# Optimization experiments

Measured on AMD Instinct MI355X. Metric: run time of the kernel, lower is better.

## Reference

```python
import jax, jax.numpy as jnp
import numpy as np

B, T, C, H = 8, 1024, 1024, 16  # batch, seq, n_embd, n_head


def setup_inputs() -> dict:
    key = jax.random.key(0)
    ks = jax.random.split(key, 5)
    scale = 1.0 / np.sqrt(C)
    return {
        "x": jax.random.normal(ks[0], (B, T, C), dtype=jnp.float32),
        "Wqkv": jax.random.normal(ks[1], (C, 3 * C), dtype=jnp.float32) * scale,
        "bqkv": jax.random.normal(ks[2], (3 * C,), dtype=jnp.float32) * 0.02,
        "Wproj": jax.random.normal(ks[3], (C, C), dtype=jnp.float32) * scale,
        "bproj": jax.random.normal(ks[4], (C,), dtype=jnp.float32) * 0.02,
        "n_head": H,
    }


def reference(x, Wqkv, bqkv, Wproj, bproj, n_head):
    Bb, Tt, Cc = x.shape
    hd = Cc // n_head  # head dim
    qkv = x @ Wqkv + bqkv                      # [B,T,3C]
    q, k, v = jnp.split(qkv, 3, axis=-1)       # each [B,T,C]
    # [B,T,C] -> [B,H,T,hd]
    def to_heads(t):
        return t.reshape(Bb, Tt, n_head, hd).transpose(0, 2, 1, 3)
    q, k, v = to_heads(q), to_heads(k), to_heads(v)
    scores = jnp.einsum("bhqd,bhkd->bhqk", q, k) / jnp.sqrt(jnp.asarray(hd, q.dtype))
    causal = jnp.tril(jnp.ones((Tt, Tt), dtype=bool))
    scores = jnp.where(causal, scores, jnp.asarray(-jnp.inf, scores.dtype))
    attn = jax.nn.softmax(scores, axis=-1)
    y = jnp.einsum("bhqk,bhkd->bhqd", attn, v)  # [B,H,T,hd]
    y = y.transpose(0, 2, 1, 3).reshape(Bb, Tt, Cc)
    return y @ Wproj + bproj
```

## Files before the change

kernel.cpp:

```cpp
#include <hip/hip_runtime.h>
#include <math.h>

#define Bz 8
#define Tz 1024
#define Cz 1024
#define Hz 16
#define HDz 64
#define Mz (Bz*Tz)
#define N1 (3*Cz)

typedef __attribute__((ext_vector_type(8))) short short8;
typedef __attribute__((ext_vector_type(4))) short short4v;
typedef __attribute__((ext_vector_type(4))) float floatx4;

__device__ __forceinline__ unsigned short f2bf(float f) {
    unsigned u = __float_as_uint(f);
    return (unsigned short)((u + 0x7FFFu + ((u >> 16) & 1u)) >> 16);
}

__device__ __forceinline__ void gload16(const void* g, void* l) {
    __builtin_amdgcn_global_load_lds(
        (const __attribute__((address_space(1))) unsigned int*)g,
        (__attribute__((address_space(3))) unsigned int*)l, 16, 0, 0);
}

__global__ __launch_bounds__(256) void cvt_kernel(const float* __restrict__ src,
    unsigned short* __restrict__ dst, int n4)
{
    int i = blockIdx.x * blockDim.x + threadIdx.x;
    if (i >= n4) return;
    float4 v = *(const float4*)&src[(size_t)i * 4];
    ushort4 o;
    o.x = f2bf(v.x); o.y = f2bf(v.y); o.z = f2bf(v.z); o.w = f2bf(v.w);
    *(ushort4*)&dst[(size_t)i * 4] = o;
}

__global__ __launch_bounds__(256) void wtrans_kernel(const float* __restrict__ W,
    unsigned short* __restrict__ Wt, int K, int N)
{
    __shared__ float tile[32][33];
    const int n0 = blockIdx.x * 32, k0 = blockIdx.y * 32;
    const int tx = threadIdx.x, ty = threadIdx.y;
#pragma unroll
    for (int i = 0; i < 4; ++i)
        tile[ty + i * 8][tx] = W[(size_t)(k0 + ty + i * 8) * N + n0 + tx];
    __syncthreads();
#pragma unroll
    for (int i = 0; i < 4; ++i)
        Wt[(size_t)(n0 + ty + i * 8) * K + k0 + tx] = f2bf(tile[tx][ty + i * 8]);
}

__global__ __launch_bounds__(256) void vtrans_kernel(const unsigned short* __restrict__ qkvb,
    unsigned short* __restrict__ Vt)
{
    __shared__ unsigned short tile[64][72];
    const int t0 = blockIdx.x * 64;
    const int bh = blockIdx.y;
    const int b = bh >> 4, h = bh & 15;
    const int tid = threadIdx.x;
#pragma unroll
    for (int it = 0; it < 2; ++it) {
        int idx = tid + it * 256;
        int tl = idx >> 3, d8 = idx & 7;
        *(short8*)&tile[tl][d8 * 8] =
            *(const short8*)&qkvb[(size_t)(b * Tz + t0 + tl) * N1 + 2 * Cz + h * HDz + d8 * 8];
    }
    __syncthreads();
#pragma unroll
    for (int it = 0; it < 2; ++it) {
        int idx = tid + it * 256;
        int d = idx >> 3, t8 = idx & 7;
        unsigned short o[8];
#pragma unroll
        for (int j = 0; j < 8; ++j) o[j] = tile[t8 * 8 + j][d];
        *(short8*)&Vt[(size_t)bh * (HDz * Tz) + (size_t)d * Tz + t0 + t8 * 8] = *(short8*)o;
    }
}

__global__ __launch_bounds__(256) void gemm_kernel(const unsigned short* __restrict__ A,
    const unsigned short* __restrict__ Bt, const float* __restrict__ bias,
    void* __restrict__ Cout, int M, int N, int K, int outBf16)
{
    __shared__ unsigned short As[128 * 64];
    __shared__ unsigned short Bs[128 * 64];
    const int tid = threadIdx.x;
    const int lane = tid & 63;
    const int w = tid >> 6, wr = w >> 1, wc = w & 1;
    const int quad = lane >> 4, m16 = lane & 15;
    const int row0 = blockIdx.y * 128, col0 = blockIdx.x * 128;

    float bv[4];
#pragma unroll
    for (int ni = 0; ni < 4; ++ni)
        bv[ni] = bias[col0 + wc * 64 + ni * 16 + m16];

    floatx4 acc[4][4];
#pragma unroll
    for (int mi = 0; mi < 4; ++mi)
#pragma unroll
        for (int ni = 0; ni < 4; ++ni)
            acc[mi][ni] = (floatx4){0.f, 0.f, 0.f, 0.f};

    const int l3 = lane >> 3;
    const int swz = ((lane & 7) ^ l3) * 8;
    const unsigned short* gA[4];
    const unsigned short* gB[4];
    unsigned short* lA[4];
    unsigned short* lB[4];
#pragma unroll
    for (int i = 0; i < 4; ++i) {
        int c = w * 4 + i;
        gA[i] = A  + (size_t)(row0 + c * 8 + l3) * K + swz;
        gB[i] = Bt + (size_t)(col0 + c * 8 + l3) * K + swz;
        lA[i] = &As[c * 512];
        lB[i] = &Bs[c * 512];
    }
    const int sw7 = m16 & 7;

    for (int k0 = 0; k0 < K; k0 += 64) {
#pragma unroll
        for (int i = 0; i < 4; ++i) {
            gload16(gA[i] + k0, lA[i]);
            gload16(gB[i] + k0, lB[i]);
        }
        __syncthreads();
#pragma unroll
        for (int s = 0; s < 2; ++s) {
            short8 af[4], bfr[4];
            const int ch = ((s * 4 + quad) ^ sw7) * 8;
#pragma unroll
            for (int mi = 0; mi < 4; ++mi)
                af[mi] = *(short8*)&As[(wr * 64 + mi * 16 + m16) * 64 + ch];
#pragma unroll
            for (int ni = 0; ni < 4; ++ni)
                bfr[ni] = *(short8*)&Bs[(wc * 64 + ni * 16 + m16) * 64 + ch];
#pragma unroll
            for (int mi = 0; mi < 4; ++mi)
#pragma unroll
                for (int ni = 0; ni < 4; ++ni)
                    acc[mi][ni] = __builtin_amdgcn_mfma_f32_16x16x32_bf16(af[mi], bfr[ni], acc[mi][ni], 0, 0, 0);
        }
        __syncthreads();
    }

#pragma unroll
    for (int mi = 0; mi < 4; ++mi)
#pragma unroll
        for (int ni = 0; ni < 4; ++ni)
#pragma unroll
            for (int reg = 0; reg < 4; ++reg) {
                int r = row0 + wr * 64 + mi * 16 + quad * 4 + reg;
                int c = col0 + wc * 64 + ni * 16 + m16;
                float v = acc[mi][ni][reg] + bv[ni];
                if (outBf16) ((unsigned short*)Cout)[(size_t)r * N + c] = f2bf(v);
                else         ((float*)Cout)[(size_t)r * N + c] = v;
            }
}

__global__ __launch_bounds__(256, 3) void attn_kernel(const unsigned short* __restrict__ qkvb,
    const unsigned short* __restrict__ VtG, unsigned short* __restrict__ attb)
{
    __shared__ unsigned short Ks[2][64 * 64];
    __shared__ unsigned short Vs[2][64 * 64];

    const int qi = (int)gridDim.x - 1 - (int)blockIdx.x;
    const int bh = blockIdx.y;
    const int b = bh >> 4, h = bh & 15;
    const int tid = threadIdx.x, lane = tid & 63, w = tid >> 6;
    const int quad = lane >> 4, m16 = lane & 15;
    const int kimax   = 2 * qi + 1;
    const int kimax_w = 2 * qi + (w >> 1);

    const unsigned short* Kb = qkvb + (size_t)(b * Tz) * N1 + Cz + h * HDz;
    const unsigned short* Vb = VtG + (size_t)bh * (HDz * Tz);

    short8 qf[2][2];
    int qrow[2];
#pragma unroll
    for (int mi = 0; mi < 2; ++mi) {
        qrow[mi] = qi * 128 + w * 32 + mi * 16 + m16;
        const size_t rq = (size_t)(b * Tz + qrow[mi]) * N1 + h * HDz;
        qf[mi][0] = *(const short8*)&qkvb[rq + quad * 8];
        qf[mi][1] = *(const short8*)&qkvb[rq + 32 + quad * 8];
    }

    floatx4 of[2][4];
#pragma unroll
    for (int mi = 0; mi < 2; ++mi)
#pragma unroll
        for (int dc = 0; dc < 4; ++dc) of[mi][dc] = (floatx4){0.f, 0.f, 0.f, 0.f};
    float psum[2] = {0.f, 0.f};

    const int l3 = lane >> 3, l7 = lane & 7;
    const int gsw = ((l7 ^ l3) << 3);
    const int r0 = w * 16 + l3, r1 = w * 16 + 8 + l3;
    const int sw = m16 & 7;
    const int p0 = (quad ^ sw) << 3;

    gload16(Kb + (size_t)r0 * N1 + gsw, &Ks[0][(2 * w) * 512]);
    gload16(Kb + (size_t)r1 * N1 + gsw, &Ks[0][(2 * w + 1) * 512]);
    gload16(Vb + (size_t)r0 * Tz + gsw, &Vs[0][(2 * w) * 512]);
    gload16(Vb + (size_t)r1 * Tz + gsw, &Vs[0][(2 * w + 1) * 512]);

    int buf = 0;
    for (int ki = 0; ki <= kimax; ++ki) {
        __syncthreads();
        if (ki < kimax) {
            int kn = (ki + 1) * 64;
            gload16(Kb + (size_t)(kn + r0) * N1 + gsw, &Ks[buf ^ 1][(2 * w) * 512]);
            gload16(Kb + (size_t)(kn + r1) * N1 + gsw, &Ks[buf ^ 1][(2 * w + 1) * 512]);
            gload16(Vb + (size_t)r0 * Tz + kn + gsw, &Vs[buf ^ 1][(2 * w) * 512]);
            gload16(Vb + (size_t)r1 * Tz + kn + gsw, &Vs[buf ^ 1][(2 * w + 1) * 512]);
        }
        if (ki <= kimax_w) {
            short8 pf[2][2];
#pragma unroll
            for (int m0 = 0; m0 < 4; ++m0) {
                const unsigned short* kr = &Ks[buf][(m0 * 16 + m16) * 64];
                short8 kf0 = *(const short8*)&kr[p0];
                short8 kf1 = *(const short8*)&kr[p0 ^ 32];
#pragma unroll
                for (int mi = 0; mi < 2; ++mi) {
                    floatx4 st = (floatx4){0.f, 0.f, 0.f, 0.f};
                    st = __builtin_amdgcn_mfma_f32_16x16x32_bf16(kf0, qf[mi][0], st, 0, 0, 0);
                    st = __builtin_amdgcn_mfma_f32_16x16x32_bf16(kf1, qf[mi][1], st, 0, 0, 0);
                    const bool needm = (ki * 64 + 63) > (qi * 128 + w * 32 + mi * 16);
#pragma unroll
                    for (int reg = 0; reg < 4; ++reg) {
                        float p = exp2f(st[reg] * 0.18033688f);
                        if (needm) {
                            int key = ki * 64 + m0 * 16 + quad * 4 + reg;
                            p = (key <= qrow[mi]) ? p : 0.f;
                        }
                        psum[mi] += p;
                        pf[mi][m0 >> 1][(m0 & 1) * 4 + reg] = (short)f2bf(p);
                    }
                }
            }
#pragma unroll
            for (int dc = 0; dc < 4; ++dc) {
                const unsigned short* vrow = &Vs[buf][(dc * 16 + m16) * 64];
#pragma unroll
                for (int kg = 0; kg < 2; ++kg) {
                    const int g0 = kg * 4 + (quad >> 1);
                    const int off = (quad & 1) * 4;
                    short4v v0 = *(const short4v*)&vrow[((g0 ^ sw) << 3) + off];
                    short4v v1 = *(const short4v*)&vrow[(((g0 + 2) ^ sw) << 3) + off];
                    short8 vf;
                    vf[0] = v0[0]; vf[1] = v0[1]; vf[2] = v0[2]; vf[3] = v0[3];
                    vf[4] = v1[0]; vf[5] = v1[1]; vf[6] = v1[2]; vf[7] = v1[3];
#pragma unroll
                    for (int mi = 0; mi < 2; ++mi)
                        of[mi][dc] = __builtin_amdgcn_mfma_f32_16x16x32_bf16(vf, pf[mi][kg], of[mi][dc], 0, 0, 0);
                }
            }
        }
        buf ^= 1;
    }

#pragma unroll
    for (int mi = 0; mi < 2; ++mi) {
        float l = psum[mi];
        l += __shfl_xor(l, 16);
        l += __shfl_xor(l, 32);
        const float inv = 1.f / l;
        const size_t orow = (size_t)(b * Tz + qrow[mi]) * Cz + h * HDz;
#pragma unroll
        for (int dc = 0; dc < 4; ++dc) {
            ushort4 o;
            o.x = f2bf(of[mi][dc][0] * inv);
            o.y = f2bf(of[mi][dc][1] * inv);
            o.z = f2bf(of[mi][dc][2] * inv);
            o.w = f2bf(of[mi][dc][3] * inv);
            *(ushort4*)&attb[orow + dc * 16 + quad * 4] = o;
        }
    }
}

extern "C" void kernel_launch(void* const* d_in, const int* in_sizes, int n_in,
                              void* d_out, int out_size, void* d_ws, size_t ws_size,
                              hipStream_t stream)
{
    const float* x     = (const float*)d_in[0];
    const float* Wqkv  = (const float*)d_in[1];
    const float* bqkv  = (const float*)d_in[2];
    const float* Wproj = (const float*)d_in[3];
    const float* bproj = (const float*)d_in[4];
    float* out = (float*)d_out;

    unsigned short* xb     = (unsigned short*)d_ws;
    unsigned short* Wqkvt  = xb + (size_t)Mz * Cz;
    unsigned short* Wprojt = Wqkvt + (size_t)N1 * Cz;
    unsigned short* qkvb   = Wprojt + (size_t)Cz * Cz;
    unsigned short* VtG    = qkvb + (size_t)Mz * N1;
    unsigned short* attb   = VtG + (size_t)(Bz * Hz) * HDz * Tz;

    cvt_kernel<<<(Mz * Cz / 4) / 256, 256, 0, stream>>>(x, xb, Mz * Cz / 4);
    wtrans_kernel<<<dim3(N1 / 32, Cz / 32), dim3(32, 8), 0, stream>>>(Wqkv, Wqkvt, Cz, N1);
    wtrans_kernel<<<dim3(Cz / 32, Cz / 32), dim3(32, 8), 0, stream>>>(Wproj, Wprojt, Cz, Cz);

    gemm_kernel<<<dim3(N1 / 128, Mz / 128), 256, 0, stream>>>(
        xb, Wqkvt, bqkv, qkvb, Mz, N1, Cz, 1);

    vtrans_kernel<<<dim3(Tz / 64, Bz * Hz), 256, 0, stream>>>(qkvb, VtG);

    attn_kernel<<<dim3(Tz / 128, Bz * Hz), 256, 0, stream>>>(qkvb, VtG, attb);

    gemm_kernel<<<dim3(Cz / 128, Mz / 128), 256, 0, stream>>>(
        attb, Wprojt, bproj, out, Mz, Cz, Cz, 0);
}
```

Baseline: 281.3 us.

## Pair complementary causal query tiles per block for balanced attention work

```diff
diff --git a/kernel.cpp b/kernel.cpp
--- a/kernel.cpp
+++ b/kernel.cpp
@@ -157,39 +157,21 @@
             }
 }
 
-__global__ __launch_bounds__(256, 3) void attn_kernel(const unsigned short* __restrict__ qkvb,
+__global__ __launch_bounds__(256) void attn_kernel(const unsigned short* __restrict__ qkvb,
     const unsigned short* __restrict__ VtG, unsigned short* __restrict__ attb)
 {
     __shared__ unsigned short Ks[2][64 * 64];
     __shared__ unsigned short Vs[2][64 * 64];
 
-    const int qi = (int)gridDim.x - 1 - (int)blockIdx.x;
+    const int bx = blockIdx.x;
     const int bh = blockIdx.y;
     const int b = bh >> 4, h = bh & 15;
     const int tid = threadIdx.x, lane = tid & 63, w = tid >> 6;
     const int quad = lane >> 4, m16 = lane & 15;
-    const int kimax   = 2 * qi + 1;
-    const int kimax_w = 2 * qi + (w >> 1);
+    const int qis[2] = {15 - bx, bx};
 
     const unsigned short* Kb = qkvb + (size_t)(b * Tz) * N1 + Cz + h * HDz;
     const unsigned short* Vb = VtG + (size_t)bh * (HDz * Tz);
-
-    short8 qf[2][2];
-    int qrow[2];
-#pragma unroll
-    for (int mi = 0; mi < 2; ++mi) {
-        qrow[mi] = qi * 128 + w * 32 + mi * 16 + m16;
-        const size_t rq = (size_t)(b * Tz + qrow[mi]) * N1 + h * HDz;
-        qf[mi][0] = *(const short8*)&qkvb[rq + quad * 8];
-        qf[mi][1] = *(const short8*)&qkvb[rq + 32 + quad * 8];
-    }
-
-    floatx4 of[2][4];
-#pragma unroll
-    for (int mi = 0; mi < 2; ++mi)
-#pragma unroll
-        for (int dc = 0; dc < 4; ++dc) of[mi][dc] = (floatx4){0.f, 0.f, 0.f, 0.f};
-    float psum[2] = {0.f, 0.f};
 
     const int l3 = lane >> 3, l7 = lane & 7;
     const int gsw = ((l7 ^ l3) << 3);
@@ -203,40 +185,50 @@
     gload16(Vb + (size_t)r1 * Tz + gsw, &Vs[0][(2 * w + 1) * 512]);
 
     int buf = 0;
-    for (int ki = 0; ki <= kimax; ++ki) {
-        __syncthreads();
-        if (ki < kimax) {
-            int kn = (ki + 1) * 64;
-            gload16(Kb + (size_t)(kn + r0) * N1 + gsw, &Ks[buf ^ 1][(2 * w) * 512]);
-            gload16(Kb + (size_t)(kn + r1) * N1 + gsw, &Ks[buf ^ 1][(2 * w + 1) * 512]);
-            gload16(Vb + (size_t)r0 * Tz + kn + gsw, &Vs[buf ^ 1][(2 * w) * 512]);
-            gload16(Vb + (size_t)r1 * Tz + kn + gsw, &Vs[buf ^ 1][(2 * w + 1) * 512]);
-        }
-        if (ki <= kimax_w) {
-            short8 pf[2][2];
+    for (int t = 0; t < 2; ++t) {
+        const int qi = qis[t];
+        const int qrow = qi * 64 + w * 16 + m16;
+
+        const size_t rq = (size_t)(b * Tz + qrow) * N1 + h * HDz;
+        const short8 qf0 = *(const short8*)&qkvb[rq + quad * 8];
+        const short8 qf1 = *(const short8*)&qkvb[rq + 32 + quad * 8];
+
+        floatx4 of[4];
+#pragma unroll
+        for (int dc = 0; dc < 4; ++dc) of[dc] = (floatx4){0.f, 0.f, 0.f, 0.f};
+        float psum = 0.f;
+
+        for (int ki = 0; ki <= qi; ++ki) {
+            __syncthreads();
+            const int nk = (ki < qi) ? (ki + 1) : (t == 0 ? 0 : -1);
+            if (nk >= 0) {
+                const size_t ko = (size_t)nk * 64;
+                gload16(Kb + (ko + r0) * N1 + gsw, &Ks[buf ^ 1][(2 * w) * 512]);
+                gload16(Kb + (ko + r1) * N1 + gsw, &Ks[buf ^ 1][(2 * w + 1) * 512]);
+                gload16(Vb + (size_t)r0 * Tz + ko + gsw, &Vs[buf ^ 1][(2 * w) * 512]);
+                gload16(Vb + (size_t)r1 * Tz + ko + gsw, &Vs[buf ^ 1][(2 * w + 1) * 512]);
+            }
+            const int diag = (ki == qi);
+
+            short8 pf[2];
 #pragma unroll
             for (int m0 = 0; m0 < 4; ++m0) {
                 const unsigned short* kr = &Ks[buf][(m0 * 16 + m16) * 64];
                 short8 kf0 = *(const short8*)&kr[p0];
                 short8 kf1 = *(const short8*)&kr[p0 ^ 32];
-#pragma unroll
-                for (int mi = 0; mi < 2; ++mi) {
-                    floatx4 st = (floatx4){0.f, 0.f, 0.f, 0.f};
-                    st = __builtin_amdgcn_mfma_f32_16x16x32_bf16(kf0, qf[mi][0], st, 0, 0, 0);
-                    st = __builtin_amdgcn_mfma_f32_16x16x32_bf16(kf1, qf[mi][1], st, 0, 0, 0);
-                    const bool needm = (ki * 64 + 63) > (qi * 128 + w * 32 + mi * 16);
-#pragma unroll
-                    for (int reg = 0; reg < 4; ++reg) {
-                        float p = exp2f(st[reg] * 0.18033688f);
-                        if (needm) {
-                            int key = ki * 64 + m0 * 16 + quad * 4 + reg;
-                            p = (key <= qrow[mi]) ? p : 0.f;
-                        }
-                        psum[mi] += p;
-                        pf[mi][m0 >> 1][(m0 & 1) * 4 + reg] = (short)f2bf(p);
-                    }
+                floatx4 st = (floatx4){0.f, 0.f, 0.f, 0.f};
+                st = __builtin_amdgcn_mfma_f32_16x16x32_bf16(kf0, qf0, st, 0, 0, 0);
+                st = __builtin_amdgcn_mfma_f32_16x16x32_bf16(kf1, qf1, st, 0, 0, 0);
+#pragma unroll
+                for (int reg = 0; reg < 4; ++reg) {
+                    float p = exp2f(st[reg] * 0.18033688f);
+                    if (diag && (m0 * 16 + quad * 4 + reg) > (w * 16 + m16))
+                        p = 0.f;
+                    psum += p;
+                    pf[m0 >> 1][(m0 & 1) * 4 + reg] = (short)f2bf(p);
                 }
             }
+
 #pragma unroll
             for (int dc = 0; dc < 4; ++dc) {
                 const unsigned short* vrow = &Vs[buf][(dc * 16 + m16) * 64];
@@ -249,29 +241,24 @@
                     short8 vf;
                     vf[0] = v0[0]; vf[1] = v0[1]; vf[2] = v0[2]; vf[3] = v0[3];
                     vf[4] = v1[0]; vf[5] = v1[1]; vf[6] = v1[2]; vf[7] = v1[3];
-#pragma unroll
-                    for (int mi = 0; mi < 2; ++mi)
-                        of[mi][dc] = __builtin_amdgcn_mfma_f32_16x16x32_bf16(vf, pf[mi][kg], of[mi][dc], 0, 0, 0);
+                    of[dc] = __builtin_amdgcn_mfma_f32_16x16x32_bf16(vf, pf[kg], of[dc], 0, 0, 0);
                 }
             }
-        }
-        buf ^= 1;
-    }
-
-#pragma unroll
-    for (int mi = 0; mi < 2; ++mi) {
-        float l = psum[mi];
+            buf ^= 1;
+        }
+
+        float l = psum;
         l += __shfl_xor(l, 16);
         l += __shfl_xor(l, 32);
         const float inv = 1.f / l;
-        const size_t orow = (size_t)(b * Tz + qrow[mi]) * Cz + h * HDz;
+        const size_t orow = (size_t)(b * Tz + qrow) * Cz + h * HDz;
 #pragma unroll
         for (int dc = 0; dc < 4; ++dc) {
             ushort4 o;
-            o.x = f2bf(of[mi][dc][0] * inv);
-            o.y = f2bf(of[mi][dc][1] * inv);
-            o.z = f2bf(of[mi][dc][2] * inv);
-            o.w = f2bf(of[mi][dc][3] * inv);
+            o.x = f2bf(of[dc][0] * inv);
+            o.y = f2bf(of[dc][1] * inv);
+            o.z = f2bf(of[dc][2] * inv);
+            o.w = f2bf(of[dc][3] * inv);
             *(ushort4*)&attb[orow + dc * 16 + quad * 4] = o;
         }
     }
@@ -304,7 +291,7 @@
 
     vtrans_kernel<<<dim3(Tz / 64, Bz * Hz), 256, 0, stream>>>(qkvb, VtG);
 
-    attn_kernel<<<dim3(Tz / 128, Bz * Hz), 256, 0, stream>>>(qkvb, VtG, attb);
+    attn_kernel<<<dim3(8, Bz * Hz), 256, 0, stream>>>(qkvb, VtG, attb);
 
     gemm_kernel<<<dim3(Cz / 128, Mz / 128), 256, 0, stream>>>(
         attb, Wprojt, bproj, out, Mz, Cz, Cz, 0);
```

Result: faster. 256.5 us (-8.8%).

## Pair causal query tiles per block and merge prep kernels into one launch

Applied to the files above, without the earlier changes.

```diff
diff --git a/kernel.cpp b/kernel.cpp
--- a/kernel.cpp
+++ b/kernel.cpp
@@ -24,23 +24,31 @@
         (__attribute__((address_space(3))) unsigned int*)l, 16, 0, 0);
 }
 
-__global__ __launch_bounds__(256) void cvt_kernel(const float* __restrict__ src,
-    unsigned short* __restrict__ dst, int n4)
-{
-    int i = blockIdx.x * blockDim.x + threadIdx.x;
-    if (i >= n4) return;
-    float4 v = *(const float4*)&src[(size_t)i * 4];
-    ushort4 o;
-    o.x = f2bf(v.x); o.y = f2bf(v.y); o.z = f2bf(v.z); o.w = f2bf(v.w);
-    *(ushort4*)&dst[(size_t)i * 4] = o;
-}
-
-__global__ __launch_bounds__(256) void wtrans_kernel(const float* __restrict__ W,
-    unsigned short* __restrict__ Wt, int K, int N)
+__global__ __launch_bounds__(256) void prep_kernel(
+    const float* __restrict__ x, unsigned short* __restrict__ xb,
+    const float* __restrict__ Wqkv, unsigned short* __restrict__ Wqkvt,
+    const float* __restrict__ Wproj, unsigned short* __restrict__ Wprojt)
 {
     __shared__ float tile[32][33];
-    const int n0 = blockIdx.x * 32, k0 = blockIdx.y * 32;
-    const int tx = threadIdx.x, ty = threadIdx.y;
+    const int bid = blockIdx.x;
+    const int tid = threadIdx.x;
+    if (bid < 8192) {
+        int i = bid * 256 + tid;
+        float4 v = *(const float4*)&x[(size_t)i * 4];
+        ushort4 o;
+        o.x = f2bf(v.x); o.y = f2bf(v.y); o.z = f2bf(v.z); o.w = f2bf(v.w);
+        *(ushort4*)&xb[(size_t)i * 4] = o;
+        return;
+    }
+    const float* W; unsigned short* Wt; int K, N, n0, k0;
+    if (bid < 11264) {
+        int b = bid - 8192;  W = Wqkv;  Wt = Wqkvt;  K = Cz; N = N1;
+        n0 = (b % 96) * 32;  k0 = (b / 96) * 32;
+    } else {
+        int b = bid - 11264; W = Wproj; Wt = Wprojt; K = Cz; N = Cz;
+        n0 = (b % 32) * 32;  k0 = (b / 32) * 32;
+    }
+    const int tx = tid & 31, ty = tid >> 5;
 #pragma unroll
     for (int i = 0; i < 4; ++i)
         tile[ty + i * 8][tx] = W[(size_t)(k0 + ty + i * 8) * N + n0 + tx];
@@ -157,65 +165,75 @@
             }
 }
 
-__global__ __launch_bounds__(256, 3) void attn_kernel(const unsigned short* __restrict__ qkvb,
+__global__ __launch_bounds__(128) void attn_kernel(const unsigned short* __restrict__ qkvb,
     const unsigned short* __restrict__ VtG, unsigned short* __restrict__ attb)
 {
     __shared__ unsigned short Ks[2][64 * 64];
     __shared__ unsigned short Vs[2][64 * 64];
 
-    const int qi = (int)gridDim.x - 1 - (int)blockIdx.x;
+    const int bx = blockIdx.x;
     const int bh = blockIdx.y;
     const int b = bh >> 4, h = bh & 15;
     const int tid = threadIdx.x, lane = tid & 63, w = tid >> 6;
     const int quad = lane >> 4, m16 = lane & 15;
-    const int kimax   = 2 * qi + 1;
-    const int kimax_w = 2 * qi + (w >> 1);
+    const int qis[2] = {15 - bx, bx};
 
     const unsigned short* Kb = qkvb + (size_t)(b * Tz) * N1 + Cz + h * HDz;
     const unsigned short* Vb = VtG + (size_t)bh * (HDz * Tz);
 
-    short8 qf[2][2];
-    int qrow[2];
-#pragma unroll
-    for (int mi = 0; mi < 2; ++mi) {
-        qrow[mi] = qi * 128 + w * 32 + mi * 16 + m16;
-        const size_t rq = (size_t)(b * Tz + qrow[mi]) * N1 + h * HDz;
-        qf[mi][0] = *(const short8*)&qkvb[rq + quad * 8];
-        qf[mi][1] = *(const short8*)&qkvb[rq + 32 + quad * 8];
-    }
-
-    floatx4 of[2][4];
-#pragma unroll
-    for (int mi = 0; mi < 2; ++mi)
-#pragma unroll
-        for (int dc = 0; dc < 4; ++dc) of[mi][dc] = (floatx4){0.f, 0.f, 0.f, 0.f};
-    float psum[2] = {0.f, 0.f};
-
     const int l3 = lane >> 3, l7 = lane & 7;
     const int gsw = ((l7 ^ l3) << 3);
-    const int r0 = w * 16 + l3, r1 = w * 16 + 8 + l3;
     const int sw = m16 & 7;
     const int p0 = (quad ^ sw) << 3;
 
-    gload16(Kb + (size_t)r0 * N1 + gsw, &Ks[0][(2 * w) * 512]);
-    gload16(Kb + (size_t)r1 * N1 + gsw, &Ks[0][(2 * w + 1) * 512]);
-    gload16(Vb + (size_t)r0 * Tz + gsw, &Vs[0][(2 * w) * 512]);
-    gload16(Vb + (size_t)r1 * Tz + gsw, &Vs[0][(2 * w + 1) * 512]);
+    int srow[4];
+#pragma unroll
+    for (int i = 0; i < 4; ++i) srow[i] = w * 32 + i * 8 + l3;
+
+#pragma unroll
+    for (int i = 0; i < 4; ++i) {
+        gload16(Kb + (size_t)srow[i] * N1 + gsw, &Ks[0][(w * 4 + i) * 512]);
+        gload16(Vb + (size_t)srow[i] * Tz + gsw, &Vs[0][(w * 4 + i) * 512]);
+    }
 
     int buf = 0;
-    for (int ki = 0; ki <= kimax; ++ki) {
-        __syncthreads();
-        if (ki < kimax) {
-            int kn = (ki + 1) * 64;
-            gload16(Kb + (size_t)(kn + r0) * N1 + gsw, &Ks[buf ^ 1][(2 * w) * 512]);
-            gload16(Kb + (size_t)(kn + r1) * N1 + gsw, &Ks[buf ^ 1][(2 * w + 1) * 512]);
-            gload16(Vb + (size_t)r0 * Tz + kn + gsw, &Vs[buf ^ 1][(2 * w) * 512]);
-            gload16(Vb + (size_t)r1 * Tz + kn + gsw, &Vs[buf ^ 1][(2 * w + 1) * 512]);
-        }
-        if (ki <= kimax_w) {
+    for (int t = 0; t < 2; ++t) {
+        const int qi = qis[t];
+
+        short8 qf[2][2];
+        int qrow[2];
+#pragma unroll
+        for (int mi = 0; mi < 2; ++mi) {
+            qrow[mi] = qi * 64 + w * 32 + mi * 16 + m16;
+            const size_t rq = (size_t)(b * Tz + qrow[mi]) * N1 + h * HDz;
+            qf[mi][0] = *(const short8*)&qkvb[rq + quad * 8];
+            qf[mi][1] = *(const short8*)&qkvb[rq + 32 + quad * 8];
+        }
+
+        floatx4 of[2][4];
+#pragma unroll
+        for (int mi = 0; mi < 2; ++mi)
+#pragma unroll
+            for (int dc = 0; dc < 4; ++dc) of[mi][dc] = (floatx4){0.f, 0.f, 0.f, 0.f};
+        float psum[2] = {0.f, 0.f};
+
+        for (int ki = 0; ki <= qi; ++ki) {
+            __syncthreads();
+            const int nk = (ki < qi) ? (ki + 1) : (t == 0 ? 0 : -1);
+            if (nk >= 0) {
+                const size_t ko = (size_t)nk * 64;
+#pragma unroll
+                for (int i = 0; i < 4; ++i) {
+                    gload16(Kb + (ko + srow[i]) * N1 + gsw, &Ks[buf ^ 1][(w * 4 + i) * 512]);
+                    gload16(Vb + (size_t)srow[i] * Tz + ko + gsw, &Vs[buf ^ 1][(w * 4 + i) * 512]);
+                }
+            }
+            const bool diag = (ki == qi);
+
             short8 pf[2][2];
 #pragma unroll
             for (int m0 = 0; m0 < 4; ++m0) {
+                if (diag && m0 * 16 > w * 32 + 31) continue;
                 const unsigned short* kr = &Ks[buf][(m0 * 16 + m16) * 64];
                 short8 kf0 = *(const short8*)&kr[p0];
                 short8 kf1 = *(const short8*)&kr[p0 ^ 32];
@@ -224,24 +242,26 @@
                     floatx4 st = (floatx4){0.f, 0.f, 0.f, 0.f};
                     st = __builtin_amdgcn_mfma_f32_16x16x32_bf16(kf0, qf[mi][0], st, 0, 0, 0);
                     st = __builtin_amdgcn_mfma_f32_16x16x32_bf16(kf1, qf[mi][1], st, 0, 0, 0);
-                    const bool needm = (ki * 64 + 63) > (qi * 128 + w * 32 + mi * 16);
 #pragma unroll
                     for (int reg = 0; reg < 4; ++reg) {
                         float p = exp2f(st[reg] * 0.18033688f);
-                        if (needm) {
-                            int key = ki * 64 + m0 * 16 + quad * 4 + reg;
-                            p = (key <= qrow[mi]) ? p : 0.f;
+                        if (diag) {
+                            int key = m0 * 16 + quad * 4 + reg;
+                            int qr  = w * 32 + mi * 16 + m16;
+                            p = (key <= qr) ? p : 0.f;
                         }
                         psum[mi] += p;
                         pf[mi][m0 >> 1][(m0 & 1) * 4 + reg] = (short)f2bf(p);
                     }
                 }
             }
+
 #pragma unroll
             for (int dc = 0; dc < 4; ++dc) {
                 const unsigned short* vrow = &Vs[buf][(dc * 16 + m16) * 64];
 #pragma unroll
                 for (int kg = 0; kg < 2; ++kg) {
+                    if (diag && kg * 32 > w * 32 + 31) continue;
                     const int g0 = kg * 4 + (quad >> 1);
                     const int off = (quad & 1) * 4;
                     short4v v0 = *(const short4v*)&vrow[((g0 ^ sw) << 3) + off];
@@ -254,25 +274,25 @@
                         of[mi][dc] = __builtin_amdgcn_mfma_f32_16x16x32_bf16(vf, pf[mi][kg], of[mi][dc], 0, 0, 0);
                 }
             }
-        }
-        buf ^= 1;
-    }
-
-#pragma unroll
-    for (int mi = 0; mi < 2; ++mi) {
-        float l = psum[mi];
-        l += __shfl_xor(l, 16);
-        l += __shfl_xor(l, 32);
-        const float inv = 1.f / l;
-        const size_t orow = (size_t)(b * Tz + qrow[mi]) * Cz + h * HDz;
-#pragma unroll
-        for (int dc = 0; dc < 4; ++dc) {
-            ushort4 o;
-            o.x = f2bf(of[mi][dc][0] * inv);
-            o.y = f2bf(of[mi][dc][1] * inv);
-            o.z = f2bf(of[mi][dc][2] * inv);
-            o.w = f2bf(of[mi][dc][3] * inv);
-            *(ushort4*)&attb[orow + dc * 16 + quad * 4] = o;
+            buf ^= 1;
+        }
+
+#pragma unroll
+        for (int mi = 0; mi < 2; ++mi) {
+            float l = psum[mi];
+            l += __shfl_xor(l, 16);
+            l += __shfl_xor(l, 32);
+            const float inv = 1.f / l;
+            const size_t orow = (size_t)(b * Tz + qrow[mi]) * Cz + h * HDz;
+#pragma unroll
+            for (int dc = 0; dc < 4; ++dc) {
+                ushort4 o;
+                o.x = f2bf(of[mi][dc][0] * inv);
+                o.y = f2bf(of[mi][dc][1] * inv);
+                o.z = f2bf(of[mi][dc][2] * inv);
+                o.w = f2bf(of[mi][dc][3] * inv);
+                *(ushort4*)&attb[orow + dc * 16 + quad * 4] = o;
+            }
         }
     }
 }
@@ -295,16 +315,14 @@
     unsigned short* VtG    = qkvb + (size_t)Mz * N1;
     unsigned short* attb   = VtG + (size_t)(Bz * Hz) * HDz * Tz;
 
-    cvt_kernel<<<(Mz * Cz / 4) / 256, 256, 0, stream>>>(x, xb, Mz * Cz / 4);
-    wtrans_kernel<<<dim3(N1 / 32, Cz / 32), dim3(32, 8), 0, stream>>>(Wqkv, Wqkvt, Cz, N1);
-    wtrans_kernel<<<dim3(Cz / 32, Cz / 32), dim3(32, 8), 0, stream>>>(Wproj, Wprojt, Cz, Cz);
+    prep_kernel<<<12288, 256, 0, stream>>>(x, xb, Wqkv, Wqkvt, Wproj, Wprojt);
 
     gemm_kernel<<<dim3(N1 / 128, Mz / 128), 256, 0, stream>>>(
         xb, Wqkvt, bqkv, qkvb, Mz, N1, Cz, 1);
 
     vtrans_kernel<<<dim3(Tz / 64, Bz * Hz), 256, 0, stream>>>(qkvb, VtG);
 
-    attn_kernel<<<dim3(Tz / 128, Bz * Hz), 256, 0, stream>>>(qkvb, VtG, attb);
+    attn_kernel<<<dim3(8, Bz * Hz), 128, 0, stream>>>(qkvb, VtG, attb);
 
     gemm_kernel<<<dim3(Cz / 128, Mz / 128), 256, 0, stream>>>(
         attb, Wprojt, bproj, out, Mz, Cz, Cz, 0);
```

Result: faster. 248.2 us (-11.8%).
